# Optimization experiments

Measured on AMD Instinct MI355X. Metric: run time of the kernel, lower is better.

## Reference

```python
import jax, jax.numpy as jnp
import numpy as np

NEG_SLOPE = 0.2  # PyG GATConv default negative_slope


def _gat_layer(x, src, dst, W, a_src, a_dst, b, heads, ch, concat, num_nodes):
    # x: [Nt, Fin]; W: [Fin, heads*ch]; a_src/a_dst: [heads, ch]
    xw = (x @ W).reshape(num_nodes, heads, ch)            # [Nt, H, C]
    alpha_s = jnp.sum(xw * a_src, axis=-1)                # [Nt, H]
    alpha_d = jnp.sum(xw * a_dst, axis=-1)                # [Nt, H]
    e = jax.nn.leaky_relu(alpha_s[src] + alpha_d[dst], NEG_SLOPE)  # [E, H]
    # segment softmax over destination nodes (every node has a self-loop)
    m = jax.lax.stop_gradient(jax.ops.segment_max(e, dst, num_segments=num_nodes))
    ex = jnp.exp(e - m[dst])
    denom = jax.ops.segment_sum(ex, dst, num_segments=num_nodes)
    alpha = ex / (denom[dst] + 1e-16)                     # [E, H]
    out = jax.ops.segment_sum(alpha[:, :, None] * xw[src], dst, num_segments=num_nodes)  # [Nt, H, C]
    out = out.reshape(num_nodes, heads * ch) if concat else out.mean(axis=1)
    return out + b


def setup_inputs() -> dict:
    key = jax.random.key(0)
    ks = jax.random.split(key, 12)
    B, N, IN, HID, H, OUT, E = 2, 10000, 256, 256, 2, 256, 160000
    x = jax.random.normal(ks[0], (B, N, IN), dtype=jnp.float32)
    edge_index = jax.random.randint(ks[1], (2, E), 0, N, dtype=jnp.int32)
    s_in = 1.0 / np.sqrt(IN)
    s_h = 1.0 / np.sqrt(HID)
    s_hh = 1.0 / np.sqrt(HID * H)
    W1 = jax.random.normal(ks[2], (IN, H * HID), dtype=jnp.float32) * s_in
    att_src1 = jax.random.normal(ks[3], (H, HID), dtype=jnp.float32) * s_h
    att_dst1 = jax.random.normal(ks[4], (H, HID), dtype=jnp.float32) * s_h
    b1 = jax.random.normal(ks[5], (H * HID,), dtype=jnp.float32) * 0.01
    W2 = jax.random.normal(ks[6], (H * HID, OUT), dtype=jnp.float32) * s_hh
    att_src2 = jax.random.normal(ks[7], (1, OUT), dtype=jnp.float32) * s_h
    att_dst2 = jax.random.normal(ks[8], (1, OUT), dtype=jnp.float32) * s_h
    b2 = jax.random.normal(ks[9], (OUT,), dtype=jnp.float32) * 0.01
    return {"x": x, "edge_index": edge_index, "W1": W1, "att_src1": att_src1,
            "att_dst1": att_dst1, "b1": b1, "W2": W2, "att_src2": att_src2,
            "att_dst2": att_dst2, "b2": b2}


def reference(x, edge_index, W1, att_src1, att_dst1, b1, W2, att_src2, att_dst2, b2):
    B, N, C = x.shape
    H, HID = att_src1.shape
    OUT = W2.shape[1]
    Nt = B * N
    xf = x.reshape(Nt, C)
    # batch edge index with per-graph node offsets (shared edges across batch)
    offs = (jnp.arange(B, dtype=edge_index.dtype) * N)       # [B]
    ei = (edge_index[:, None, :] + offs[None, :, None]).reshape(2, -1)  # [2, B*E]
    # add self loops (PyG GATConv default)
    loops = jnp.arange(Nt, dtype=edge_index.dtype)
    src = jnp.concatenate([ei[0], loops])
    dst = jnp.concatenate([ei[1], loops])
    h = _gat_layer(xf, src, dst, W1, att_src1, att_dst1, b1, H, HID, True, Nt)
    h = jax.nn.gelu(h, approximate=False)  # torch F.gelu default = exact erf
    out = _gat_layer(h, src, dst, W2, att_src2, att_dst2, b2, 1, OUT, False, Nt)
    return out.reshape(B, N, OUT)
```

## Files before the change

kernel.cpp:

```cpp
#include <hip/hip_runtime.h>
#include <math.h>

constexpr int B_   = 2;
constexpr int N_   = 10000;
constexpr int IN_  = 256;
constexpr int HID_ = 256;
constexpr int H1_  = 2;
constexpr int OUT_ = 256;
constexpr int E_   = 160000;
constexpr int NT_  = B_ * N_;
constexpr float SLOPE = 0.2f;
constexpr int DMAX = 128;

typedef unsigned short u16;
typedef __attribute__((ext_vector_type(8))) short short8;
typedef __attribute__((ext_vector_type(4))) float f32x4;

__device__ __forceinline__ u16 f2bf(float f) {
    unsigned int u = __float_as_uint(f);
    u += 0x7fffu + ((u >> 16) & 1u);
    return (u16)(u >> 16);
}
__device__ __forceinline__ void bf8(uint4 r, float4& lo, float4& hi) {
    lo = make_float4(__uint_as_float((r.x & 0xffffu) << 16),
                     __uint_as_float(r.x & 0xffff0000u),
                     __uint_as_float((r.y & 0xffffu) << 16),
                     __uint_as_float(r.y & 0xffff0000u));
    hi = make_float4(__uint_as_float((r.z & 0xffffu) << 16),
                     __uint_as_float(r.z & 0xffff0000u),
                     __uint_as_float((r.w & 0xffffu) << 16),
                     __uint_as_float(r.w & 0xffff0000u));
}
__device__ __forceinline__ void fma4(float4& a, float s, float4 v) {
    a.x = fmaf(s, v.x, a.x); a.y = fmaf(s, v.y, a.y);
    a.z = fmaf(s, v.z, a.z); a.w = fmaf(s, v.w, a.w);
}
__device__ __forceinline__ float lrelu(float e) { return (e < 0.f) ? SLOPE * e : e; }

__device__ __forceinline__ void g2l16(const void* g, void* l) {
    __builtin_amdgcn_global_load_lds(
        (const __attribute__((address_space(1))) unsigned int*)g,
        (__attribute__((address_space(3))) unsigned int*)l, 16, 0, 0);
}

__global__ __launch_bounds__(256) void k_wprep(
    const float* __restrict__ W1,
    const float* __restrict__ aS1, const float* __restrict__ aD1,
    const float* __restrict__ W2,
    const float* __restrict__ aS2, const float* __restrict__ aD2,
    float* __restrict__ w1s, float* __restrict__ w1d,
    float* __restrict__ w2s, float* __restrict__ w2d,
    u16* __restrict__ W1t, u16* __restrict__ W2t,
    uint4* __restrict__ zbase) {
    __shared__ float tld[32][33];
    const int blk = blockIdx.x;
    if (blk < 16) {
        for (int i = blk * 256 + threadIdx.x; i < 12500; i += 16 * 256)
            zbase[i] = make_uint4(0, 0, 0, 0);
    } else if (blk < 528) {
        int wv = (blk - 16) * 4 + (threadIdx.x >> 6);
        int lane = threadIdx.x & 63;
        int c = lane * 4;
        float4 wr, av;
        if (wv < 1024) {
            int h = (wv >> 8) & 1;
            int k = wv & 255;
            const float* a = (wv < 512) ? aS1 : aD1;
            wr = *(const float4*)(W1 + (size_t)k * 512 + h * 256 + c);
            av = *(const float4*)(a + h * 256 + c);
        } else {
            int k = (wv - 1024) & 511;
            const float* a = (wv < 1536) ? aS2 : aD2;
            wr = *(const float4*)(W2 + (size_t)k * 256 + c);
            av = *(const float4*)(a + c);
        }
        float s = wr.x * av.x + wr.y * av.y + wr.z * av.z + wr.w * av.w;
        #pragma unroll
        for (int off = 32; off; off >>= 1) s += __shfl_down(s, off);
        if (lane == 0) {
            if (wv < 512)       w1s[wv] = s;
            else if (wv < 1024) w1d[wv - 512] = s;
            else if (wv < 1536) w2s[wv - 1024] = s;
            else                w2d[wv - 1536] = s;
        }
    } else {
        const int b = blk - 528;
        const int z = b >> 7;
        const int bb = b & 127;
        const float* S = z ? W2 : W1;
        u16* D = z ? W2t : W1t;
        const int R = z ? 512 : 256;
        const int C = z ? 256 : 512;
        const int xt = C >> 5;
        const int bx = bb % xt, by = bb / xt;
        const int tx = threadIdx.x & 31, ty = threadIdx.x >> 5;
        int xx = bx * 32 + tx;
        int y0 = by * 32 + ty;
        #pragma unroll
        for (int i = 0; i < 32; i += 8)
            tld[ty + i][tx] = S[(size_t)(y0 + i) * C + xx];
        __syncthreads();
        int xo = by * 32 + tx;
        int yo = bx * 32 + ty;
        #pragma unroll
        for (int i = 0; i < 32; i += 8)
            D[(size_t)(yo + i) * R + xo] = f2bf(tld[tx][ty + i]);
    }
}

__global__ __launch_bounds__(256) void k_pre(
    const float* __restrict__ x, u16* __restrict__ Xb,
    const float* __restrict__ w1s, const float* __restrict__ w1d,
    float* __restrict__ as1, float* __restrict__ ad1,
    const int* __restrict__ ei, int* __restrict__ cnt, int* __restrict__ bucket) {
    const int NB = NT_ / 4;
    if ((int)blockIdx.x < NB) {
        const int w = threadIdx.x >> 6, lane = threadIdx.x & 63;
        const int nt = blockIdx.x * 4 + w;
        const int c = lane * 4;
        float4 v = *(const float4*)(x + (size_t)nt * 256 + c);
        ((uint2*)(Xb + (size_t)nt * 256))[lane] =
            make_uint2((unsigned)f2bf(v.x) | ((unsigned)f2bf(v.y) << 16),
                       (unsigned)f2bf(v.z) | ((unsigned)f2bf(v.w) << 16));
        float4 s0v = *(const float4*)(w1s + c);
        float4 s1v = *(const float4*)(w1s + 256 + c);
        float4 d0v = *(const float4*)(w1d + c);
        float4 d1v = *(const float4*)(w1d + 256 + c);
        float s0 = v.x*s0v.x + v.y*s0v.y + v.z*s0v.z + v.w*s0v.w;
        float s1 = v.x*s1v.x + v.y*s1v.y + v.z*s1v.z + v.w*s1v.w;
        float d0 = v.x*d0v.x + v.y*d0v.y + v.z*d0v.z + v.w*d0v.w;
        float d1 = v.x*d1v.x + v.y*d1v.y + v.z*d1v.z + v.w*d1v.w;
        #pragma unroll
        for (int off = 32; off; off >>= 1) {
            s0 += __shfl_down(s0, off); s1 += __shfl_down(s1, off);
            d0 += __shfl_down(d0, off); d1 += __shfl_down(d1, off);
        }
        if (lane == 0) {
            as1[nt * 2] = s0; as1[nt * 2 + 1] = s1;
            ad1[nt * 2] = d0; ad1[nt * 2 + 1] = d1;
        }
    } else {
        int e = (blockIdx.x - NB) * 256 + threadIdx.x;
        if (e < E_) {
            int s = ei[e], d = ei[E_ + e];
            int p = atomicAdd(&cnt[d], 1);
            if (p < DMAX - 1) bucket[d * DMAX + p] = s;
        }
    }
}

__global__ __launch_bounds__(256) void k_agg1x(
    const u16* __restrict__ Xb,
    const float* __restrict__ as_, const float* __restrict__ ad_,
    const int* __restrict__ cnt, const int* __restrict__ bucket,
    u16* __restrict__ Y) {
    __shared__ int   stl[4][DMAX];
    __shared__ float exw[4][2 * DMAX];
    const int w    = threadIdx.x >> 6;
    const int lane = threadIdx.x & 63;
    const int half = lane >> 5;
    const int l32  = lane & 31;
    const int nt   = blockIdx.x * 4 + w;
    if (nt >= NT_) return;
    const int nl   = nt % N_;
    const int boff = nt - nl;
    const int r0   = nl * DMAX;
    int deg = cnt[nl]; deg = (deg < DMAX - 1) ? deg : (DMAX - 1);
    const float adv0 = ad_[nt * 2], adv1 = ad_[nt * 2 + 1];
    const float adv = half ? adv1 : adv0;

    for (int i = lane; i <= deg; i += 64)
        stl[w][i] = (i < deg) ? (bucket[r0 + i] + boff) : nt;

    float den = 0.f;
    for (int i = l32; i <= deg; i += 32) {
        int st = stl[w][i];
        float ex = __expf(lrelu(as_[st * 2 + half] + adv));
        exw[w][2 * i + half] = ex;
        den += ex;
    }
    #pragma unroll
    for (int off = 16; off; off >>= 1) den += __shfl_xor(den, off);
    const float inv = 1.f / (den + 1e-16f);
    const float invO = __shfl_xor(inv, 32);

    const int slot = half;
    const int nin = deg + 1;
    const u16* fb = Xb + l32 * 8;
    float4 A0l = {0,0,0,0}, A0h = {0,0,0,0}, A1l = {0,0,0,0}, A1h = {0,0,0,0};
    float4 B0l = {0,0,0,0}, B0h = {0,0,0,0}, B1l = {0,0,0,0}, B1h = {0,0,0,0};
    int j = 0;
    for (; j + 8 <= nin; j += 8) {
        int sA = stl[w][j + slot],     sB = stl[w][j + 2 + slot];
        int sC = stl[w][j + 4 + slot], sD = stl[w][j + 6 + slot];
        float2 wA = *(const float2*)&exw[w][2 * (j + slot)];
        float2 wB = *(const float2*)&exw[w][2 * (j + 2 + slot)];
        float2 wC = *(const float2*)&exw[w][2 * (j + 4 + slot)];
        float2 wD = *(const float2*)&exw[w][2 * (j + 6 + slot)];
        uint4 vA = *(const uint4*)(fb + (size_t)sA * 256);
        uint4 vB = *(const uint4*)(fb + (size_t)sB * 256);
        uint4 vC = *(const uint4*)(fb + (size_t)sC * 256);
        uint4 vD = *(const uint4*)(fb + (size_t)sD * 256);
        float4 lo, hi;
        bf8(vA, lo, hi); fma4(A0l, wA.x, lo); fma4(A0h, wA.x, hi);
                         fma4(A1l, wA.y, lo); fma4(A1h, wA.y, hi);
        bf8(vB, lo, hi); fma4(B0l, wB.x, lo); fma4(B0h, wB.x, hi);
                         fma4(B1l, wB.y, lo); fma4(B1h, wB.y, hi);
        bf8(vC, lo, hi); fma4(A0l, wC.x, lo); fma4(A0h, wC.x, hi);
                         fma4(A1l, wC.y, lo); fma4(A1h, wC.y, hi);
        bf8(vD, lo, hi); fma4(B0l, wD.x, lo); fma4(B0h, wD.x, hi);
                         fma4(B1l, wD.y, lo); fma4(B1h, wD.y, hi);
    }
    for (int jj = j + slot; jj < nin; jj += 2) {
        int s0 = stl[w][jj];
        float2 w01 = *(const float2*)&exw[w][2 * jj];
        uint4 v0 = *(const uint4*)(fb + (size_t)s0 * 256);
        float4 lo, hi;
        bf8(v0, lo, hi); fma4(A0l, w01.x, lo); fma4(A0h, w01.x, hi);
                         fma4(A1l, w01.y, lo); fma4(A1h, w01.y, hi);
    }
    A0l.x += B0l.x; A0l.y += B0l.y; A0l.z += B0l.z; A0l.w += B0l.w;
    A0h.x += B0h.x; A0h.y += B0h.y; A0h.z += B0h.z; A0h.w += B0h.w;
    A1l.x += B1l.x; A1l.y += B1l.y; A1l.z += B1l.z; A1l.w += B1l.w;
    A1h.x += B1h.x; A1h.y += B1h.y; A1h.z += B1h.z; A1h.w += B1h.w;
    A0l.x += __shfl_xor(A0l.x, 32); A0l.y += __shfl_xor(A0l.y, 32);
    A0l.z += __shfl_xor(A0l.z, 32); A0l.w += __shfl_xor(A0l.w, 32);
    A0h.x += __shfl_xor(A0h.x, 32); A0h.y += __shfl_xor(A0h.y, 32);
    A0h.z += __shfl_xor(A0h.z, 32); A0h.w += __shfl_xor(A0h.w, 32);
    A1l.x += __shfl_xor(A1l.x, 32); A1l.y += __shfl_xor(A1l.y, 32);
    A1l.z += __shfl_xor(A1l.z, 32); A1l.w += __shfl_xor(A1l.w, 32);
    A1h.x += __shfl_xor(A1h.x, 32); A1h.y += __shfl_xor(A1h.y, 32);
    A1h.z += __shfl_xor(A1h.z, 32); A1h.w += __shfl_xor(A1h.w, 32);

    if (slot == 0) {
        float f0[8] = { A0l.x*inv,  A0l.y*inv,  A0l.z*inv,  A0l.w*inv,
                        A0h.x*inv,  A0h.y*inv,  A0h.z*inv,  A0h.w*inv };
        float f1[8] = { A1l.x*invO, A1l.y*invO, A1l.z*invO, A1l.w*invO,
                        A1h.x*invO, A1h.y*invO, A1h.z*invO, A1h.w*invO };
        size_t ob = (size_t)nt * 512 + l32 * 8;
        *(uint4*)(Y + ob) =
            make_uint4((unsigned)f2bf(f0[0]) | ((unsigned)f2bf(f0[1]) << 16),
                       (unsigned)f2bf(f0[2]) | ((unsigned)f2bf(f0[3]) << 16),
                       (unsigned)f2bf(f0[4]) | ((unsigned)f2bf(f0[5]) << 16),
                       (unsigned)f2bf(f0[6]) | ((unsigned)f2bf(f0[7]) << 16));
        *(uint4*)(Y + ob + 256) =
            make_uint4((unsigned)f2bf(f1[0]) | ((unsigned)f2bf(f1[1]) << 16),
                       (unsigned)f2bf(f1[2]) | ((unsigned)f2bf(f1[3]) << 16),
                       (unsigned)f2bf(f1[4]) | ((unsigned)f2bf(f1[5]) << 16),
                       (unsigned)f2bf(f1[6]) | ((unsigned)f2bf(f1[7]) << 16));
    }
}

__global__ __launch_bounds__(256) void gemm_g(
    const u16* __restrict__ Yf, const u16* __restrict__ W1t,
    u16* __restrict__ Hb,
    const float* __restrict__ b1,
    const float* __restrict__ w2s, const float* __restrict__ w2d,
    float* __restrict__ as2, float* __restrict__ ad2, int M) {
    __shared__ u16 sA[128 * 32], sB[128 * 32];
    const int tid = threadIdx.x, wave = tid >> 6, lane = tid & 63;
    const int bm = blockIdx.x, bn = blockIdx.y, h = blockIdx.z;
    const int srow = 16 * wave + (lane >> 2);
    const int kc   = (lane & 3) * 8;
    int rA0 = bm * 128 + srow;       int rA1 = rA0 + 64;
    rA0 = (rA0 < M) ? rA0 : (M - 1); rA1 = (rA1 < M) ? rA1 : (M - 1);
    const int rB0 = bn * 128 + srow; const int rB1 = rB0 + 64;
    const u16* gA0 = Yf + (size_t)rA0 * 512 + h * 256 + kc;
    const u16* gA1 = Yf + (size_t)rA1 * 512 + h * 256 + kc;
    const u16* gB0 = W1t + (size_t)(h * 256 + rB0) * 256 + kc;
    const u16* gB1 = W1t + (size_t)(h * 256 + rB1) * 256 + kc;
    u16* lA0 = sA + wave * 512;  u16* lA1 = lA0 + 2048;
    u16* lB0 = sB + wave * 512;  u16* lB1 = lB0 + 2048;

    const int wm = wave & 1, wn = wave >> 1;
    const int l15 = lane & 15, quad = lane >> 4;
    const int aOff = (wm * 64 + l15) * 32 + quad * 8;
    const int bOff = (wn * 64 + l15) * 32 + quad * 8;

    f32x4 acc[4][4];
    #pragma unroll
    for (int i = 0; i < 4; i++)
        #pragma unroll
        for (int j = 0; j < 4; j++)
            acc[i][j] = (f32x4){0.f, 0.f, 0.f, 0.f};

    for (int k0 = 0; k0 < 256; k0 += 32) {
        g2l16(gA0 + k0, lA0); g2l16(gA1 + k0, lA1);
        g2l16(gB0 + k0, lB0); g2l16(gB1 + k0, lB1);
        __syncthreads();
        short8 af[4], bf[4];
        #pragma unroll
        for (int i = 0; i < 4; i++) {
            af[i] = *(const short8*)(sA + aOff + i * 512);
            bf[i] = *(const short8*)(sB + bOff + i * 512);
        }
        #pragma unroll
        for (int i = 0; i < 4; i++)
            #pragma unroll
            for (int j = 0; j < 4; j++)
                acc[i][j] = __builtin_amdgcn_mfma_f32_16x16x32_bf16(af[i], bf[j], acc[i][j], 0, 0, 0);
        __syncthreads();
    }

    const int colL = bn * 128 + wn * 64;
    float Bv[4], Sv[4], Dv[4];
    #pragma unroll
    for (int j = 0; j < 4; j++) {
        int cg = h * 256 + colL + j * 16 + l15;
        Bv[j] = b1[cg]; Sv[j] = w2s[cg]; Dv[j] = w2d[cg];
    }
    #pragma unroll
    for (int i = 0; i < 4; i++) {
        #pragma unroll
        for (int r = 0; r < 4; r++) {
            int row = bm * 128 + wm * 64 + i * 16 + quad * 4 + r;
            float o[4], ps = 0.f, pd = 0.f;
            #pragma unroll
            for (int j = 0; j < 4; j++) {
                float v = acc[i][j][r] + Bv[j];
                v = 0.5f * v * (1.f + erff(v * 0.70710678118654752f));
                o[j] = v;
                ps = fmaf(v, Sv[j], ps);
                pd = fmaf(v, Dv[j], pd);
            }
            #pragma unroll
            for (int off = 1; off < 16; off <<= 1) {
                ps += __shfl_xor(ps, off);
                pd += __shfl_xor(pd, off);
            }
            if (row < M) {
                if (l15 == 0) { atomicAdd(&as2[row], ps); atomicAdd(&ad2[row], pd); }
                #pragma unroll
                for (int j = 0; j < 4; j++)
                    Hb[(size_t)row * 512 + h * 256 + colL + j * 16 + l15] = f2bf(o[j]);
            }
        }
    }
}

__global__ __launch_bounds__(256) void gemm_p(
    const u16* __restrict__ A, const u16* __restrict__ Bt,
    u16* __restrict__ C16, int M, int N, int K) {
    __shared__ u16 sA[64 * 32], sB[128 * 32];
    const int tid = threadIdx.x, wave = tid >> 6, lane = tid & 63;
    const int bm = blockIdx.x, bn = blockIdx.y;
    const int srow = 16 * wave + (lane >> 2);
    const int kc   = (lane & 3) * 8;
    int rA = bm * 64 + srow;  rA = (rA < M) ? rA : (M - 1);
    const int rB0 = bn * 128 + srow; const int rB1 = rB0 + 64;
    const u16* gA  = A  + (size_t)rA  * K + kc;
    const u16* gB0 = Bt + (size_t)rB0 * K + kc;
    const u16* gB1 = Bt + (size_t)rB1 * K + kc;
    u16* lA  = sA + wave * 512;
    u16* lB0 = sB + wave * 512;  u16* lB1 = lB0 + 2048;

    const int wm = wave & 1, wn = wave >> 1;
    const int l15 = lane & 15, quad = lane >> 4;
    const int aOff = (wm * 32 + l15) * 32 + quad * 8;
    const int bOff = (wn * 64 + l15) * 32 + quad * 8;

    f32x4 acc[2][4];
    #pragma unroll
    for (int i = 0; i < 2; i++)
        #pragma unroll
        for (int j = 0; j < 4; j++)
            acc[i][j] = (f32x4){0.f, 0.f, 0.f, 0.f};

    for (int k0 = 0; k0 < K; k0 += 32) {
        g2l16(gA + k0, lA);
        g2l16(gB0 + k0, lB0); g2l16(gB1 + k0, lB1);
        __syncthreads();
        short8 af[2], bf[4];
        #pragma unroll
        for (int i = 0; i < 2; i++)
            af[i] = *(const short8*)(sA + aOff + i * 512);
        #pragma unroll
        for (int j = 0; j < 4; j++)
            bf[j] = *(const short8*)(sB + bOff + j * 512);
        #pragma unroll
        for (int i = 0; i < 2; i++)
            #pragma unroll
            for (int j = 0; j < 4; j++)
                acc[i][j] = __builtin_amdgcn_mfma_f32_16x16x32_bf16(af[i], bf[j], acc[i][j], 0, 0, 0);
        __syncthreads();
    }
    #pragma unroll
    for (int i = 0; i < 2; i++) {
        #pragma unroll
        for (int r = 0; r < 4; r++) {
            int row = bm * 64 + wm * 32 + i * 16 + quad * 4 + r;
            if (row < M) {
                #pragma unroll
                for (int j = 0; j < 4; j++) {
                    int col = bn * 128 + wn * 64 + j * 16 + l15;
                    C16[(size_t)row * N + col] = f2bf(acc[i][j][r]);
                }
            }
        }
    }
}

__global__ __launch_bounds__(256) void k_agg_h1(
    const u16* __restrict__ feat,
    const float* __restrict__ as_, const float* __restrict__ ad_,
    const int* __restrict__ cnt, const int* __restrict__ bucket,
    const float* __restrict__ bias,
    float* __restrict__ out) {
    __shared__ int   stl[4][DMAX];
    __shared__ float exw[4][DMAX];
    const int w    = threadIdx.x >> 6;
    const int lane = threadIdx.x & 63;
    const int slot = lane >> 5;
    const int l32  = lane & 31;
    const int nt   = blockIdx.x * 4 + w;
    if (nt >= NT_) return;
    const int nl   = nt % N_;
    const int boff = nt - nl;
    const int r0   = nl * DMAX;
    int deg = cnt[nl]; deg = (deg < DMAX - 1) ? deg : (DMAX - 1);
    const float adv = ad_[nt];

    for (int i = lane; i <= deg; i += 64)
        stl[w][i] = (i < deg) ? (bucket[r0 + i] + boff) : nt;

    float den = 0.f;
    for (int i = lane; i <= deg; i += 64) {
        int st = stl[w][i];
        float ex = __expf(lrelu(as_[st] + adv));
        exw[w][i] = ex;
        den += ex;
    }
    #pragma unroll
    for (int off = 32; off; off >>= 1) den += __shfl_xor(den, off);
    const float inv = 1.f / (den + 1e-16f);

    const int nin = deg + 1;
    const u16* fb = feat + l32 * 8;
    float4 aA0 = {0,0,0,0}, aB0 = {0,0,0,0}, aA1 = {0,0,0,0}, aB1 = {0,0,0,0};
    int j = 0;
    for (; j + 8 <= nin; j += 8) {
        int sA = stl[w][j + slot],     sB = stl[w][j + 2 + slot];
        int sC = stl[w][j + 4 + slot], sD = stl[w][j + 6 + slot];
        float wA = exw[w][j + slot],     wB = exw[w][j + 2 + slot];
        float wC = exw[w][j + 4 + slot], wD = exw[w][j + 6 + slot];
        uint4 vA = *(const uint4*)(fb + (size_t)sA * 256);
        uint4 vB = *(const uint4*)(fb + (size_t)sB * 256);
        uint4 vC = *(const uint4*)(fb + (size_t)sC * 256);
        uint4 vD = *(const uint4*)(fb + (size_t)sD * 256);
        float4 lo, hi;
        bf8(vA, lo, hi); fma4(aA0, wA, lo); fma4(aB0, wA, hi);
        bf8(vB, lo, hi); fma4(aA1, wB, lo); fma4(aB1, wB, hi);
        bf8(vC, lo, hi); fma4(aA0, wC, lo); fma4(aB0, wC, hi);
        bf8(vD, lo, hi); fma4(aA1, wD, lo); fma4(aB1, wD, hi);
    }
    for (; j + 4 <= nin; j += 4) {
        int sA = stl[w][j + slot], sB = stl[w][j + 2 + slot];
        float wA = exw[w][j + slot], wB = exw[w][j + 2 + slot];
        uint4 vA = *(const uint4*)(fb + (size_t)sA * 256);
        uint4 vB = *(const uint4*)(fb + (size_t)sB * 256);
        float4 lo, hi;
        bf8(vA, lo, hi); fma4(aA0, wA, lo); fma4(aB0, wA, hi);
        bf8(vB, lo, hi); fma4(aA1, wB, lo); fma4(aB1, wB, hi);
    }
    for (int jj = j + slot; jj < nin; jj += 2) {
        int s0 = stl[w][jj];
        float w0 = exw[w][jj];
        uint4 v0 = *(const uint4*)(fb + (size_t)s0 * 256);
        float4 lo, hi;
        bf8(v0, lo, hi); fma4(aA0, w0, lo); fma4(aB0, w0, hi);
    }
    aA0.x += aA1.x; aA0.y += aA1.y; aA0.z += aA1.z; aA0.w += aA1.w;
    aB0.x += aB1.x; aB0.y += aB1.y; aB0.z += aB1.z; aB0.w += aB1.w;
    aA0.x += __shfl_xor(aA0.x, 32); aA0.y += __shfl_xor(aA0.y, 32);
    aA0.z += __shfl_xor(aA0.z, 32); aA0.w += __shfl_xor(aA0.w, 32);
    aB0.x += __shfl_xor(aB0.x, 32); aB0.y += __shfl_xor(aB0.y, 32);
    aB0.z += __shfl_xor(aB0.z, 32); aB0.w += __shfl_xor(aB0.w, 32);

    if (slot == 0) {
        int c = l32 * 8;
        float4 b0 = *(const float4*)(bias + c);
        float4 b1 = *(const float4*)(bias + c + 4);
        float* ob = out + (size_t)nt * 256 + c;
        *(float4*)(ob)     = make_float4(aA0.x * inv + b0.x, aA0.y * inv + b0.y,
                                         aA0.z * inv + b0.z, aA0.w * inv + b0.w);
        *(float4*)(ob + 4) = make_float4(aB0.x * inv + b1.x, aB0.y * inv + b1.y,
                                         aB0.z * inv + b1.z, aB0.w * inv + b1.w);
    }
}

extern "C" void kernel_launch(void* const* d_in, const int* in_sizes, int n_in,
                              void* d_out, int out_size, void* d_ws, size_t ws_size,
                              hipStream_t stream) {
    const float* x    = (const float*)d_in[0];
    const int*   ei   = (const int*)  d_in[1];
    const float* W1   = (const float*)d_in[2];
    const float* aS1  = (const float*)d_in[3];
    const float* aD1  = (const float*)d_in[4];
    const float* b1   = (const float*)d_in[5];
    const float* W2   = (const float*)d_in[6];
    const float* aS2  = (const float*)d_in[7];
    const float* aD2  = (const float*)d_in[8];
    const float* b2   = (const float*)d_in[9];
    float* out = (float*)d_out;

    u16* Xb   = (u16*)d_ws;
    u16* Y    = Xb + (size_t)NT_ * 256;
    u16* Hb   = Y  + (size_t)NT_ * 512;
    u16* hw16 = Hb + (size_t)NT_ * 512;
    float* as1 = (float*)(hw16 + (size_t)NT_ * 256);
    float* ad1 = as1 + NT_ * H1_;
    float* as2 = ad1 + NT_ * H1_;
    float* ad2 = as2 + NT_;
    int* cnt   = (int*)(ad2 + NT_);
    int* bucket= cnt + N_;
    u16* W1t   = (u16*)(bucket + N_ * DMAX);
    u16* W2t   = W1t + 512 * 256;
    float* w1s = (float*)(W2t + 256 * 512);
    float* w1d = w1s + 512;
    float* w2s = w1d + 512;
    float* w2d = w2s + 512;

    k_wprep<<<784, 256, 0, stream>>>(W1, aS1, aD1, W2, aS2, aD2,
                                     w1s, w1d, w2s, w2d, W1t, W2t, (uint4*)as2);

    k_pre<<<NT_ / 4 + (E_ + 255) / 256, 256, 0, stream>>>(
        x, Xb, w1s, w1d, as1, ad1, ei, cnt, bucket);

    k_agg1x<<<(NT_ + 3) / 4, 256, 0, stream>>>(Xb, as1, ad1, cnt, bucket, Y);
    gemm_g<<<dim3((NT_ + 127) / 128, 2, 2), 256, 0, stream>>>(
        Y, W1t, Hb, b1, w2s, w2d, as2, ad2, NT_);

    gemm_p<<<dim3((NT_ + 63) / 64, OUT_ / 128), 256, 0, stream>>>(
        Hb, W2t, hw16, NT_, OUT_, H1_ * HID_);
    k_agg_h1<<<(NT_ + 3) / 4, 256, 0, stream>>>(hw16, as2, ad2, cnt, bucket, b2, out);
}
```

Baseline: 184.0 us.

## Retile both GEMMs to 64x64 blocks with K=64 steps and XOR-swizzled LDS

Both MFMA GEMMs (the fused GELU/attention-logit projection and the second-layer projection) now use 64x64 output tiles with a 64-wide K step. LDS reads and writes use an XOR swizzle to avoid bank conflicts, and launch bounds request six blocks per CU. The grids grow to match the smaller tiles. This is meant to raise occupancy and reduce LDS conflicts, at the cost of less data reuse per tile and more redundant global loads of A and B.

```diff
diff --git a/kernel.cpp b/kernel.cpp
--- a/kernel.cpp
+++ b/kernel.cpp
@@ -230,7 +230,7 @@
     A1l.x += __shfl_xor(A1l.x, 32); A1l.y += __shfl_xor(A1l.y, 32);
     A1l.z += __shfl_xor(A1l.z, 32); A1l.w += __shfl_xor(A1l.w, 32);
     A1h.x += __shfl_xor(A1h.x, 32); A1h.y += __shfl_xor(A1h.y, 32);
-    A1h.z += __shfl_xor(A1h.z, 32); A1h.w += __shfl_xor(A1h.w, 32);
+    A1h.w += __shfl_xor(A1h.w, 32); A1h.z += __shfl_xor(A1h.z, 32);
 
     if (slot == 0) {
         float f0[8] = { A0l.x*inv,  A0l.y*inv,  A0l.z*inv,  A0l.w*inv,
@@ -251,72 +251,83 @@
     }
 }
 
-__global__ __launch_bounds__(256) void gemm_g(
+__global__ __launch_bounds__(256, 6) void gemm_g(
     const u16* __restrict__ Yf, const u16* __restrict__ W1t,
     u16* __restrict__ Hb,
     const float* __restrict__ b1,
     const float* __restrict__ w2s, const float* __restrict__ w2d,
     float* __restrict__ as2, float* __restrict__ ad2, int M) {
-    __shared__ u16 sA[128 * 32], sB[128 * 32];
+    __shared__ u16 sA[64 * 64], sB[64 * 64];
     const int tid = threadIdx.x, wave = tid >> 6, lane = tid & 63;
     const int bm = blockIdx.x, bn = blockIdx.y, h = blockIdx.z;
-    const int srow = 16 * wave + (lane >> 2);
-    const int kc   = (lane & 3) * 8;
-    int rA0 = bm * 128 + srow;       int rA1 = rA0 + 64;
-    rA0 = (rA0 < M) ? rA0 : (M - 1); rA1 = (rA1 < M) ? rA1 : (M - 1);
-    const int rB0 = bn * 128 + srow; const int rB1 = rB0 + 64;
+
+    const int rsel = lane >> 3;
+    const int kc   = ((lane & 7) ^ rsel) * 8;
+    int rA0 = bm * 64 + wave * 16 + rsel;
+    int rA1 = rA0 + 8;
+    rA0 = (rA0 < M) ? rA0 : (M - 1);
+    rA1 = (rA1 < M) ? rA1 : (M - 1);
+    const int rB = bn * 64 + wave * 16 + rsel;
     const u16* gA0 = Yf + (size_t)rA0 * 512 + h * 256 + kc;
     const u16* gA1 = Yf + (size_t)rA1 * 512 + h * 256 + kc;
-    const u16* gB0 = W1t + (size_t)(h * 256 + rB0) * 256 + kc;
-    const u16* gB1 = W1t + (size_t)(h * 256 + rB1) * 256 + kc;
-    u16* lA0 = sA + wave * 512;  u16* lA1 = lA0 + 2048;
-    u16* lB0 = sB + wave * 512;  u16* lB1 = lB0 + 2048;
+    const u16* gB0 = W1t + (size_t)(h * 256 + rB) * 256 + kc;
+    const u16* gB1 = W1t + (size_t)(h * 256 + rB + 8) * 256 + kc;
+    u16* lA0 = sA + wave * 1024; u16* lA1 = lA0 + 512;
+    u16* lB0 = sB + wave * 1024; u16* lB1 = lB0 + 512;
 
     const int wm = wave & 1, wn = wave >> 1;
     const int l15 = lane & 15, quad = lane >> 4;
-    const int aOff = (wm * 64 + l15) * 32 + quad * 8;
-    const int bOff = (wn * 64 + l15) * 32 + quad * 8;
-
-    f32x4 acc[4][4];
-    #pragma unroll
-    for (int i = 0; i < 4; i++)
-        #pragma unroll
-        for (int j = 0; j < 4; j++)
+    const int sw  = l15 & 7;
+    const int aR0 = (wm * 32 + l15) * 64; const int aR1 = aR0 + 1024;
+    const int bR0 = (wn * 32 + l15) * 64; const int bR1 = bR0 + 1024;
+    const int c0 = (quad ^ sw) * 8;
+    const int c1 = ((4 + quad) ^ sw) * 8;
+
+    f32x4 acc[2][2];
+    #pragma unroll
+    for (int i = 0; i < 2; i++)
+        #pragma unroll
+        for (int j = 0; j < 2; j++)
             acc[i][j] = (f32x4){0.f, 0.f, 0.f, 0.f};
 
-    for (int k0 = 0; k0 < 256; k0 += 32) {
+    for (int k0 = 0; k0 < 256; k0 += 64) {
         g2l16(gA0 + k0, lA0); g2l16(gA1 + k0, lA1);
         g2l16(gB0 + k0, lB0); g2l16(gB1 + k0, lB1);
         __syncthreads();
-        short8 af[4], bf[4];
-        #pragma unroll
-        for (int i = 0; i < 4; i++) {
-            af[i] = *(const short8*)(sA + aOff + i * 512);
-            bf[i] = *(const short8*)(sB + bOff + i * 512);
-        }
-        #pragma unroll
-        for (int i = 0; i < 4; i++)
-            #pragma unroll
-            for (int j = 0; j < 4; j++)
-                acc[i][j] = __builtin_amdgcn_mfma_f32_16x16x32_bf16(af[i], bf[j], acc[i][j], 0, 0, 0);
+        short8 a0 = *(const short8*)(sA + aR0 + c0);
+        short8 a1 = *(const short8*)(sA + aR1 + c0);
+        short8 b0 = *(const short8*)(sB + bR0 + c0);
+        short8 b1v = *(const short8*)(sB + bR1 + c0);
+        acc[0][0] = __builtin_amdgcn_mfma_f32_16x16x32_bf16(a0, b0, acc[0][0], 0, 0, 0);
+        acc[0][1] = __builtin_amdgcn_mfma_f32_16x16x32_bf16(a0, b1v, acc[0][1], 0, 0, 0);
+        acc[1][0] = __builtin_amdgcn_mfma_f32_16x16x32_bf16(a1, b0, acc[1][0], 0, 0, 0);
+        acc[1][1] = __builtin_amdgcn_mfma_f32_16x16x32_bf16(a1, b1v, acc[1][1], 0, 0, 0);
+        a0 = *(const short8*)(sA + aR0 + c1);
+        a1 = *(const short8*)(sA + aR1 + c1);
+        b0 = *(const short8*)(sB + bR0 + c1);
+        b1v = *(const short8*)(sB + bR1 + c1);
+        acc[0][0] = __builtin_amdgcn_mfma_f32_16x16x32_bf16(a0, b0, acc[0][0], 0, 0, 0);
+        acc[0][1] = __builtin_amdgcn_mfma_f32_16x16x32_bf16(a0, b1v, acc[0][1], 0, 0, 0);
+        acc[1][0] = __builtin_amdgcn_mfma_f32_16x16x32_bf16(a1, b0, acc[1][0], 0, 0, 0);
+        acc[1][1] = __builtin_amdgcn_mfma_f32_16x16x32_bf16(a1, b1v, acc[1][1], 0, 0, 0);
         __syncthreads();
     }
 
-    const int colL = bn * 128 + wn * 64;
-    float Bv[4], Sv[4], Dv[4];
-    #pragma unroll
-    for (int j = 0; j < 4; j++) {
+    const int colL = bn * 64 + wn * 32;
+    float Bv[2], Sv[2], Dv[2];
+    #pragma unroll
+    for (int j = 0; j < 2; j++) {
         int cg = h * 256 + colL + j * 16 + l15;
         Bv[j] = b1[cg]; Sv[j] = w2s[cg]; Dv[j] = w2d[cg];
     }
     #pragma unroll
-    for (int i = 0; i < 4; i++) {
+    for (int i = 0; i < 2; i++) {
         #pragma unroll
         for (int r = 0; r < 4; r++) {
-            int row = bm * 128 + wm * 64 + i * 16 + quad * 4 + r;
-            float o[4], ps = 0.f, pd = 0.f;
+            int row = bm * 64 + wm * 32 + i * 16 + quad * 4 + r;
+            float o[2], ps = 0.f, pd = 0.f;
             #pragma unroll
-            for (int j = 0; j < 4; j++) {
+            for (int j = 0; j < 2; j++) {
                 float v = acc[i][j][r] + Bv[j];
                 v = 0.5f * v * (1.f + erff(v * 0.70710678118654752f));
                 o[j] = v;
@@ -331,57 +342,69 @@
             if (row < M) {
                 if (l15 == 0) { atomicAdd(&as2[row], ps); atomicAdd(&ad2[row], pd); }
                 #pragma unroll
-                for (int j = 0; j < 4; j++)
+                for (int j = 0; j < 2; j++)
                     Hb[(size_t)row * 512 + h * 256 + colL + j * 16 + l15] = f2bf(o[j]);
             }
         }
     }
 }
 
-__global__ __launch_bounds__(256) void gemm_p(
+__global__ __launch_bounds__(256, 6) void gemm_p(
     const u16* __restrict__ A, const u16* __restrict__ Bt,
     u16* __restrict__ C16, int M, int N, int K) {
-    __shared__ u16 sA[64 * 32], sB[128 * 32];
+    __shared__ u16 sA[64 * 64], sB[64 * 64];
     const int tid = threadIdx.x, wave = tid >> 6, lane = tid & 63;
     const int bm = blockIdx.x, bn = blockIdx.y;
-    const int srow = 16 * wave + (lane >> 2);
-    const int kc   = (lane & 3) * 8;
-    int rA = bm * 64 + srow;  rA = (rA < M) ? rA : (M - 1);
-    const int rB0 = bn * 128 + srow; const int rB1 = rB0 + 64;
-    const u16* gA  = A  + (size_t)rA  * K + kc;
-    const u16* gB0 = Bt + (size_t)rB0 * K + kc;
-    const u16* gB1 = Bt + (size_t)rB1 * K + kc;
-    u16* lA  = sA + wave * 512;
-    u16* lB0 = sB + wave * 512;  u16* lB1 = lB0 + 2048;
+
+    const int rsel = lane >> 3;
+    const int kc   = ((lane & 7) ^ rsel) * 8;
+    int rA0 = bm * 64 + wave * 16 + rsel;
+    int rA1 = rA0 + 8;
+    rA0 = (rA0 < M) ? rA0 : (M - 1);
+    rA1 = (rA1 < M) ? rA1 : (M - 1);
+    const int rB = bn * 64 + wave * 16 + rsel;
+    const u16* gA0 = A + (size_t)rA0 * K + kc;
+    const u16* gA1 = A + (size_t)rA1 * K + kc;
+    const u16* gB0 = Bt + (size_t)rB * K + kc;
+    const u16* gB1 = Bt + (size_t)(rB + 8) * K + kc;
+    u16* lA0 = sA + wave * 1024; u16* lA1 = lA0 + 512;
+    u16* lB0 = sB + wave * 1024; u16* lB1 = lB0 + 512;
 
     const int wm = wave & 1, wn = wave >> 1;
     const int l15 = lane & 15, quad = lane >> 4;
-    const int aOff = (wm * 32 + l15) * 32 + quad * 8;
-    const int bOff = (wn * 64 + l15) * 32 + quad * 8;
-
-    f32x4 acc[2][4];
+    const int sw  = l15 & 7;
+    const int aR0 = (wm * 32 + l15) * 64; const int aR1 = aR0 + 1024;
+    const int bR0 = (wn * 32 + l15) * 64; const int bR1 = bR0 + 1024;
+    const int c0 = (quad ^ sw) * 8;
+    const int c1 = ((4 + quad) ^ sw) * 8;
+
+    f32x4 acc[2][2];
     #pragma unroll
     for (int i = 0; i < 2; i++)
         #pragma unroll
-        for (int j = 0; j < 4; j++)
+        for (int j = 0; j < 2; j++)
             acc[i][j] = (f32x4){0.f, 0.f, 0.f, 0.f};
 
-    for (int k0 = 0; k0 < K; k0 += 32) {
-        g2l16(gA + k0, lA);
+    for (int k0 = 0; k0 < K; k0 += 64) {
+        g2l16(gA0 + k0, lA0); g2l16(gA1 + k0, lA1);
         g2l16(gB0 + k0, lB0); g2l16(gB1 + k0, lB1);
         __syncthreads();
-        short8 af[2], bf[4];
-        #pragma unroll
-        for (int i = 0; i < 2; i++)
-            af[i] = *(const short8*)(sA + aOff + i * 512);
-        #pragma unroll
-        for (int j = 0; j < 4; j++)
-            bf[j] = *(const short8*)(sB + bOff + j * 512);
-        #pragma unroll
-        for (int i = 0; i < 2; i++)
-            #pragma unroll
-            for (int j = 0; j < 4; j++)
-                acc[i][j] = __builtin_amdgcn_mfma_f32_16x16x32_bf16(af[i], bf[j], acc[i][j], 0, 0, 0);
+        short8 a0 = *(const short8*)(sA + aR0 + c0);
+        short8 a1 = *(const short8*)(sA + aR1 + c0);
+        short8 b0 = *(const short8*)(sB + bR0 + c0);
+        short8 b1v = *(const short8*)(sB + bR1 + c0);
+        acc[0][0] = __builtin_amdgcn_mfma_f32_16x16x32_bf16(a0, b0, acc[0][0], 0, 0, 0);
+        acc[0][1] = __builtin_amdgcn_mfma_f32_16x16x32_bf16(a0, b1v, acc[0][1], 0, 0, 0);
+        acc[1][0] = __builtin_amdgcn_mfma_f32_16x16x32_bf16(a1, b0, acc[1][0], 0, 0, 0);
+        acc[1][1] = __builtin_amdgcn_mfma_f32_16x16x32_bf16(a1, b1v, acc[1][1], 0, 0, 0);
+        a0 = *(const short8*)(sA + aR0 + c1);
+        a1 = *(const short8*)(sA + aR1 + c1);
+        b0 = *(const short8*)(sB + bR0 + c1);
+        b1v = *(const short8*)(sB + bR1 + c1);
+        acc[0][0] = __builtin_amdgcn_mfma_f32_16x16x32_bf16(a0, b0, acc[0][0], 0, 0, 0);
+        acc[0][1] = __builtin_amdgcn_mfma_f32_16x16x32_bf16(a0, b1v, acc[0][1], 0, 0, 0);
+        acc[1][0] = __builtin_amdgcn_mfma_f32_16x16x32_bf16(a1, b0, acc[1][0], 0, 0, 0);
+        acc[1][1] = __builtin_amdgcn_mfma_f32_16x16x32_bf16(a1, b1v, acc[1][1], 0, 0, 0);
         __syncthreads();
     }
     #pragma unroll
@@ -391,8 +414,8 @@
             int row = bm * 64 + wm * 32 + i * 16 + quad * 4 + r;
             if (row < M) {
                 #pragma unroll
-                for (int j = 0; j < 4; j++) {
-                    int col = bn * 128 + wn * 64 + j * 16 + l15;
+                for (int j = 0; j < 2; j++) {
+                    int col = bn * 64 + wn * 32 + j * 16 + l15;
                     C16[(size_t)row * N + col] = f2bf(acc[i][j][r]);
                 }
             }
@@ -527,10 +550,10 @@
         x, Xb, w1s, w1d, as1, ad1, ei, cnt, bucket);
 
     k_agg1x<<<(NT_ + 3) / 4, 256, 0, stream>>>(Xb, as1, ad1, cnt, bucket, Y);
-    gemm_g<<<dim3((NT_ + 127) / 128, 2, 2), 256, 0, stream>>>(
+    gemm_g<<<dim3((NT_ + 63) / 64, 4, 2), 256, 0, stream>>>(
         Y, W1t, Hb, b1, w2s, w2d, as2, ad2, NT_);
 
-    gemm_p<<<dim3((NT_ + 63) / 64, OUT_ / 128), 256, 0, stream>>>(
+    gemm_p<<<dim3((NT_ + 63) / 64, OUT_ / 64), 256, 0, stream>>>(
         Hb, W2t, hw16, NT_, OUT_, H1_ * HID_);
     k_agg_h1<<<(NT_ + 3) / 4, 256, 0, stream>>>(hw16, as2, ad2, cnt, bucket, b2, out);
 }
```

After: 187.5 us. No clear change (+1.9%).

## Feed MFMA operands straight from global memory in both GEMMs, dropping LDS staging

Applied to the files above, without the earlier changes.

Both bf16 GEMM kernels stop staging tiles in shared memory through global_load_lds and barriers. Each wave now loads its A and B fragments directly from global memory into registers and runs the MFMAs on them. Tiles are reshaped so each block covers 128 rows by 64 columns, with each wave owning 32 rows, and the launch grids and occupancy hints change to match. This removes barrier stalls and LDS traffic, but B tiles are now re-read by every wave through the cache, and the global reads are less well coalesced. It also adds a harmless dummy variable in the aggregation loop.

```diff
diff --git a/kernel.cpp b/kernel.cpp
--- a/kernel.cpp
+++ b/kernel.cpp
@@ -36,12 +36,6 @@
     a.z = fmaf(s, v.z, a.z); a.w = fmaf(s, v.w, a.w);
 }
 __device__ __forceinline__ float lrelu(float e) { return (e < 0.f) ? SLOPE * e : e; }
-
-__device__ __forceinline__ void g2l16(const void* g, void* l) {
-    __builtin_amdgcn_global_load_lds(
-        (const __attribute__((address_space(1))) unsigned int*)g,
-        (__attribute__((address_space(3))) unsigned int*)l, 16, 0, 0);
-}
 
 __global__ __launch_bounds__(256) void k_wprep(
     const float* __restrict__ W1,
@@ -251,69 +245,60 @@
     }
 }
 
-__global__ __launch_bounds__(256) void gemm_g(
+__global__ __launch_bounds__(256, 4) void gemm_g(
     const u16* __restrict__ Yf, const u16* __restrict__ W1t,
     u16* __restrict__ Hb,
     const float* __restrict__ b1,
     const float* __restrict__ w2s, const float* __restrict__ w2d,
     float* __restrict__ as2, float* __restrict__ ad2, int M) {
-    __shared__ u16 sA[128 * 32], sB[128 * 32];
     const int tid = threadIdx.x, wave = tid >> 6, lane = tid & 63;
     const int bm = blockIdx.x, bn = blockIdx.y, h = blockIdx.z;
-    const int srow = 16 * wave + (lane >> 2);
-    const int kc   = (lane & 3) * 8;
-    int rA0 = bm * 128 + srow;       int rA1 = rA0 + 64;
-    rA0 = (rA0 < M) ? rA0 : (M - 1); rA1 = (rA1 < M) ? rA1 : (M - 1);
-    const int rB0 = bn * 128 + srow; const int rB1 = rB0 + 64;
-    const u16* gA0 = Yf + (size_t)rA0 * 512 + h * 256 + kc;
-    const u16* gA1 = Yf + (size_t)rA1 * 512 + h * 256 + kc;
-    const u16* gB0 = W1t + (size_t)(h * 256 + rB0) * 256 + kc;
-    const u16* gB1 = W1t + (size_t)(h * 256 + rB1) * 256 + kc;
-    u16* lA0 = sA + wave * 512;  u16* lA1 = lA0 + 2048;
-    u16* lB0 = sB + wave * 512;  u16* lB1 = lB0 + 2048;
-
-    const int wm = wave & 1, wn = wave >> 1;
-    const int l15 = lane & 15, quad = lane >> 4;
-    const int aOff = (wm * 64 + l15) * 32 + quad * 8;
-    const int bOff = (wn * 64 + l15) * 32 + quad * 8;
-
-    f32x4 acc[4][4];
-    #pragma unroll
-    for (int i = 0; i < 4; i++)
+    const int l15 = lane & 15, q = lane >> 4;
+
+    const int rb = bm * 128 + wave * 32;
+    int r0 = rb + l15;      r0 = (r0 < M) ? r0 : (M - 1);
+    int r1 = rb + 16 + l15; r1 = (r1 < M) ? r1 : (M - 1);
+    const u16* a0p = Yf + (size_t)r0 * 512 + h * 256 + q * 8;
+    const u16* a1p = Yf + (size_t)r1 * 512 + h * 256 + q * 8;
+    const int cb = bn * 64;
+    const u16* bp = W1t + (size_t)(h * 256 + cb + l15) * 256 + q * 8;
+
+    f32x4 acc[2][4];
+    #pragma unroll
+    for (int i = 0; i < 2; i++)
         #pragma unroll
         for (int j = 0; j < 4; j++)
             acc[i][j] = (f32x4){0.f, 0.f, 0.f, 0.f};
 
-    for (int k0 = 0; k0 < 256; k0 += 32) {
-        g2l16(gA0 + k0, lA0); g2l16(gA1 + k0, lA1);
-        g2l16(gB0 + k0, lB0); g2l16(gB1 + k0, lB1);
-        __syncthreads();
-        short8 af[4], bf[4];
-        #pragma unroll
-        for (int i = 0; i < 4; i++) {
-            af[i] = *(const short8*)(sA + aOff + i * 512);
-            bf[i] = *(const short8*)(sB + bOff + i * 512);
-        }
-        #pragma unroll
-        for (int i = 0; i < 4; i++)
-            #pragma unroll
-            for (int j = 0; j < 4; j++)
-                acc[i][j] = __builtin_amdgcn_mfma_f32_16x16x32_bf16(af[i], bf[j], acc[i][j], 0, 0, 0);
-        __syncthreads();
-    }
-
-    const int colL = bn * 128 + wn * 64;
+    #pragma unroll 4
+    for (int kk = 0; kk < 256; kk += 32) {
+        short8 a0 = *(const short8*)(a0p + kk);
+        short8 a1 = *(const short8*)(a1p + kk);
+        short8 b0 = *(const short8*)(bp + kk);
+        short8 b1 = *(const short8*)(bp + 16 * 256 + kk);
+        short8 b2 = *(const short8*)(bp + 32 * 256 + kk);
+        short8 b3 = *(const short8*)(bp + 48 * 256 + kk);
+        acc[0][0] = __builtin_amdgcn_mfma_f32_16x16x32_bf16(a0, b0, acc[0][0], 0, 0, 0);
+        acc[0][1] = __builtin_amdgcn_mfma_f32_16x16x32_bf16(a0, b1, acc[0][1], 0, 0, 0);
+        acc[0][2] = __builtin_amdgcn_mfma_f32_16x16x32_bf16(a0, b2, acc[0][2], 0, 0, 0);
+        acc[0][3] = __builtin_amdgcn_mfma_f32_16x16x32_bf16(a0, b3, acc[0][3], 0, 0, 0);
+        acc[1][0] = __builtin_amdgcn_mfma_f32_16x16x32_bf16(a1, b0, acc[1][0], 0, 0, 0);
+        acc[1][1] = __builtin_amdgcn_mfma_f32_16x16x32_bf16(a1, b1, acc[1][1], 0, 0, 0);
+        acc[1][2] = __builtin_amdgcn_mfma_f32_16x16x32_bf16(a1, b2, acc[1][2], 0, 0, 0);
+        acc[1][3] = __builtin_amdgcn_mfma_f32_16x16x32_bf16(a1, b3, acc[1][3], 0, 0, 0);
+    }
+
     float Bv[4], Sv[4], Dv[4];
     #pragma unroll
     for (int j = 0; j < 4; j++) {
-        int cg = h * 256 + colL + j * 16 + l15;
+        int cg = h * 256 + cb + j * 16 + l15;
         Bv[j] = b1[cg]; Sv[j] = w2s[cg]; Dv[j] = w2d[cg];
     }
     #pragma unroll
-    for (int i = 0; i < 4; i++) {
+    for (int i = 0; i < 2; i++) {
         #pragma unroll
         for (int r = 0; r < 4; r++) {
-            int row = bm * 128 + wm * 64 + i * 16 + quad * 4 + r;
+            int row = rb + i * 16 + q * 4 + r;
             float o[4], ps = 0.f, pd = 0.f;
             #pragma unroll
             for (int j = 0; j < 4; j++) {
@@ -332,32 +317,27 @@
                 if (l15 == 0) { atomicAdd(&as2[row], ps); atomicAdd(&ad2[row], pd); }
                 #pragma unroll
                 for (int j = 0; j < 4; j++)
-                    Hb[(size_t)row * 512 + h * 256 + colL + j * 16 + l15] = f2bf(o[j]);
+                    Hb[(size_t)row * 512 + h * 256 + cb + j * 16 + l15] = f2bf(o[j]);
             }
         }
     }
 }
 
-__global__ __launch_bounds__(256) void gemm_p(
+__global__ __launch_bounds__(256, 4) void gemm_p(
     const u16* __restrict__ A, const u16* __restrict__ Bt,
     u16* __restrict__ C16, int M, int N, int K) {
-    __shared__ u16 sA[64 * 32], sB[128 * 32];
     const int tid = threadIdx.x, wave = tid >> 6, lane = tid & 63;
     const int bm = blockIdx.x, bn = blockIdx.y;
-    const int srow = 16 * wave + (lane >> 2);
-    const int kc   = (lane & 3) * 8;
-    int rA = bm * 64 + srow;  rA = (rA < M) ? rA : (M - 1);
-    const int rB0 = bn * 128 + srow; const int rB1 = rB0 + 64;
-    const u16* gA  = A  + (size_t)rA  * K + kc;
-    const u16* gB0 = Bt + (size_t)rB0 * K + kc;
-    const u16* gB1 = Bt + (size_t)rB1 * K + kc;
-    u16* lA  = sA + wave * 512;
-    u16* lB0 = sB + wave * 512;  u16* lB1 = lB0 + 2048;
-
-    const int wm = wave & 1, wn = wave >> 1;
-    const int l15 = lane & 15, quad = lane >> 4;
-    const int aOff = (wm * 32 + l15) * 32 + quad * 8;
-    const int bOff = (wn * 64 + l15) * 32 + quad * 8;
+    const int l15 = lane & 15, q = lane >> 4;
+
+    const int rb = bm * 128 + wave * 32;
+    int r0 = rb + l15;      r0 = (r0 < M) ? r0 : (M - 1);
+    int r1 = rb + 16 + l15; r1 = (r1 < M) ? r1 : (M - 1);
+    const u16* a0p = A + (size_t)r0 * K + q * 8;
+    const u16* a1p = A + (size_t)r1 * K + q * 8;
+    const int cb = bn * 64;
+    const u16* bp = Bt + (size_t)(cb + l15) * K + q * 8;
+    const size_t bstride = (size_t)16 * K;
 
     f32x4 acc[2][4];
     #pragma unroll
@@ -366,35 +346,32 @@
         for (int j = 0; j < 4; j++)
             acc[i][j] = (f32x4){0.f, 0.f, 0.f, 0.f};
 
-    for (int k0 = 0; k0 < K; k0 += 32) {
-        g2l16(gA + k0, lA);
-        g2l16(gB0 + k0, lB0); g2l16(gB1 + k0, lB1);
-        __syncthreads();
-        short8 af[2], bf[4];
-        #pragma unroll
-        for (int i = 0; i < 2; i++)
-            af[i] = *(const short8*)(sA + aOff + i * 512);
-        #pragma unroll
-        for (int j = 0; j < 4; j++)
-            bf[j] = *(const short8*)(sB + bOff + j * 512);
-        #pragma unroll
-        for (int i = 0; i < 2; i++)
-            #pragma unroll
-            for (int j = 0; j < 4; j++)
-                acc[i][j] = __builtin_amdgcn_mfma_f32_16x16x32_bf16(af[i], bf[j], acc[i][j], 0, 0, 0);
-        __syncthreads();
+    #pragma unroll 4
+    for (int kk = 0; kk < K; kk += 32) {
+        short8 a0 = *(const short8*)(a0p + kk);
+        short8 a1 = *(const short8*)(a1p + kk);
+        short8 b0 = *(const short8*)(bp + kk);
+        short8 b1 = *(const short8*)(bp + bstride + kk);
+        short8 b2 = *(const short8*)(bp + 2 * bstride + kk);
+        short8 b3 = *(const short8*)(bp + 3 * bstride + kk);
+        acc[0][0] = __builtin_amdgcn_mfma_f32_16x16x32_bf16(a0, b0, acc[0][0], 0, 0, 0);
+        acc[0][1] = __builtin_amdgcn_mfma_f32_16x16x32_bf16(a0, b1, acc[0][1], 0, 0, 0);
+        acc[0][2] = __builtin_amdgcn_mfma_f32_16x16x32_bf16(a0, b2, acc[0][2], 0, 0, 0);
+        acc[0][3] = __builtin_amdgcn_mfma_f32_16x16x32_bf16(a0, b3, acc[0][3], 0, 0, 0);
+        acc[1][0] = __builtin_amdgcn_mfma_f32_16x16x32_bf16(a1, b0, acc[1][0], 0, 0, 0);
+        acc[1][1] = __builtin_amdgcn_mfma_f32_16x16x32_bf16(a1, b1, acc[1][1], 0, 0, 0);
+        acc[1][2] = __builtin_amdgcn_mfma_f32_16x16x32_bf16(a1, b2, acc[1][2], 0, 0, 0);
+        acc[1][3] = __builtin_amdgcn_mfma_f32_16x16x32_bf16(a1, b3, acc[1][3], 0, 0, 0);
     }
     #pragma unroll
     for (int i = 0; i < 2; i++) {
         #pragma unroll
         for (int r = 0; r < 4; r++) {
-            int row = bm * 64 + wm * 32 + i * 16 + quad * 4 + r;
+            int row = rb + i * 16 + q * 4 + r;
             if (row < M) {
                 #pragma unroll
-                for (int j = 0; j < 4; j++) {
-                    int col = bn * 128 + wn * 64 + j * 16 + l15;
-                    C16[(size_t)row * N + col] = f2bf(acc[i][j][r]);
-                }
+                for (int j = 0; j < 4; j++)
+                    C16[(size_t)row * N + cb + j * 16 + l15] = f2bf(acc[i][j][r]);
             }
         }
     }
@@ -441,8 +418,10 @@
     for (; j + 8 <= nin; j += 8) {
         int sA = stl[w][j + slot],     sB = stl[w][j + 2 + slot];
         int sC = stl[w][j + 4 + slot], sD = stl[w][j + 6 + slot];
-        float wA = exw[w][j + slot],     wB = exw[w][j + 2 + slot];
+        float wA = exw[w][j + slot],     float_wB = 0.f;
+        float wB = exw[w][j + 2 + slot];
         float wC = exw[w][j + 4 + slot], wD = exw[w][j + 6 + slot];
+        (void)float_wB;
         uint4 vA = *(const uint4*)(fb + (size_t)sA * 256);
         uint4 vB = *(const uint4*)(fb + (size_t)sB * 256);
         uint4 vC = *(const uint4*)(fb + (size_t)sC * 256);
@@ -527,10 +506,10 @@
         x, Xb, w1s, w1d, as1, ad1, ei, cnt, bucket);
 
     k_agg1x<<<(NT_ + 3) / 4, 256, 0, stream>>>(Xb, as1, ad1, cnt, bucket, Y);
-    gemm_g<<<dim3((NT_ + 127) / 128, 2, 2), 256, 0, stream>>>(
+    gemm_g<<<dim3((NT_ + 127) / 128, 4, 2), 256, 0, stream>>>(
         Y, W1t, Hb, b1, w2s, w2d, as2, ad2, NT_);
 
-    gemm_p<<<dim3((NT_ + 63) / 64, OUT_ / 128), 256, 0, stream>>>(
+    gemm_p<<<dim3((NT_ + 127) / 128, OUT_ / 64), 256, 0, stream>>>(
         Hb, W2t, hw16, NT_, OUT_, H1_ * HID_);
     k_agg_h1<<<(NT_ + 3) / 4, 256, 0, stream>>>(hw16, as2, ad2, cnt, bucket, b2, out);
 }
```

Result: slower. 216.4 us (+17.6%).
